# Optimization experiments

Hardware: AMD Instinct MI355X
Metric: run time of the kernel (lower is better)

Reference implementation:

```python
import jax, jax.numpy as jnp
import numpy as np

NUM_VIEW = 300
NUM_ANGLE = 12
NUM_DEPTH = 4
GRASP_MAX_WIDTH = 0.1
B, C, NS, NG = 2, 512, 2048, 2000


def generate_grasp_views(N=NUM_VIEW):
    phi = (np.sqrt(5.0) - 1.0) / 2.0  # fibonacci sphere
    idxs = jnp.arange(N, dtype=jnp.float32)
    Z = (2.0 * idxs + 1.0) / N - 1.0
    r = jnp.sqrt(jnp.maximum(1.0 - Z * Z, 0.0))
    X = r * jnp.cos(2.0 * jnp.pi * idxs * phi)
    Y = r * jnp.sin(2.0 * jnp.pi * idxs * phi)
    return jnp.stack([X, Y, Z], -1)  # [N,3]


def viewpoint_params_to_matrix(towards, angle):
    # towards [...,3], angle [...]
    ax = towards
    zero = jnp.zeros_like(ax[..., 0])
    ay = jnp.stack([-ax[..., 1], ax[..., 0], zero], -1)
    ynorm = jnp.linalg.norm(ay, axis=-1, keepdims=True)
    ay = jnp.where(ynorm == 0, jnp.array([0.0, 1.0, 0.0], ax.dtype), ay)
    ax = ax / jnp.linalg.norm(ax, axis=-1, keepdims=True)
    ay = ay / jnp.linalg.norm(ay, axis=-1, keepdims=True)
    az = jnp.cross(ax, ay)
    c, s = jnp.cos(angle), jnp.sin(angle)
    one = jnp.ones_like(c)
    R1 = jnp.stack([one, zero * 0 + jnp.zeros_like(c), jnp.zeros_like(c),
                    jnp.zeros_like(c), c, -s,
                    jnp.zeros_like(c), s, c], -1).reshape(angle.shape + (3, 3))
    R2 = jnp.stack([ax, ay, az], -1)  # axes as columns
    return R2 @ R1


def conv1d(x, w, b):
    # 1x1 Conv1d == channel matmul. x [B,Ci,N], w [Co,Ci]
    return jnp.einsum('oi,bin->bon', w, x) + b[None, :, None]


def knn1(q, ref):
    # K=1 nearest neighbor indices of q [Nq,3] in ref [Nr,3]
    d = (jnp.sum(q * q, -1, keepdims=True) + jnp.sum(ref * ref, -1)[None, :]
         - 2.0 * q @ ref.T)
    return jnp.argmin(d, axis=-1)


def normalize_tensor(t, eps=1e-8):
    mx = jnp.max(t, -1, keepdims=True)
    mn = jnp.min(t, -1, keepdims=True)
    return (t - mn) / (mx - mn + eps)


def _process_one(seed_xyz, pose, gpoints, gscores, gwidths, views, views_rot):
    R, t = pose[:, :3], pose[:, 3]
    gp_trans = gpoints @ R.T + t                      # [Ng,3]
    gv_trans = views @ R.T                            # [V,3]
    gv_rot_trans = jnp.einsum('ij,vjk->vik', R, views_rot)  # [V,3,3]
    view_inds = knn1(views, gv_trans)                 # [V]
    gv_rot_trans = gv_rot_trans[view_inds]            # [V,3,3]
    nn_inds = knn1(seed_xyz, gp_trans)                # [Ns]
    gp_out = gp_trans[nn_inds]                        # [Ns,3]
    # gather seed dim first (Ns<Ng) then reindex views; axes independent
    sc = gscores[nn_inds][:, view_inds]               # [Ns,V,A,D]
    wd = gwidths[nn_inds][:, view_inds]
    rot = jnp.broadcast_to(gv_rot_trans[None], (seed_xyz.shape[0],) + gv_rot_trans.shape)
    return gp_out, rot, sc, wd


def setup_inputs() -> dict:
    key = jax.random.key(0)
    ks = jax.random.split(key, 16)
    seed_features = jax.random.normal(ks[0], (B, C, NS), jnp.float32)
    point_clouds = jax.random.normal(ks[1], (B, NS, 3), jnp.float32) * 0.2
    Rq = np.linalg.qr(np.asarray(jax.random.normal(ks[2], (B, 3, 3))))[0].astype(np.float32)
    trans = jax.random.normal(ks[3], (B, 3, 1), jnp.float32) * 0.1
    object_pose = jnp.concatenate([jnp.asarray(Rq), trans], -1)  # [B,3,4]
    grasp_points = jax.random.normal(ks[4], (B, NG, 3), jnp.float32) * 0.2
    grasp_labels = jax.random.uniform(ks[5], (B, NG, NUM_VIEW, NUM_ANGLE, NUM_DEPTH)) * 1.2 - 0.2
    grasp_offsets = jax.random.uniform(ks[6], (B, NG, NUM_VIEW, NUM_ANGLE, NUM_DEPTH)) * 0.15
    w = lambda k, co, ci: jax.random.normal(k, (co, ci), jnp.float32) * 0.05
    bz = lambda co: jnp.zeros((co,), jnp.float32)
    return {
        'seed_features': seed_features, 'point_clouds': point_clouds,
        'object_pose': object_pose, 'grasp_points': grasp_points,
        'grasp_labels': grasp_labels, 'grasp_offsets': grasp_offsets,
        'aw1_w': w(ks[7], C, C), 'aw1_b': bz(C),
        'aw2_w': w(ks[8], C, C), 'aw2_b': bz(C),
        'aw3_w': w(ks[9], NUM_VIEW, C), 'aw3_b': bz(NUM_VIEW),
        'sw1_w': w(ks[10], C, C), 'sw1_b': bz(C),
        'sw2_w': w(ks[11], NUM_DEPTH * NUM_ANGLE * 2, C), 'sw2_b': bz(NUM_DEPTH * NUM_ANGLE * 2),
    }


def reference(seed_features, point_clouds, object_pose, grasp_points,
              grasp_labels, grasp_offsets, aw1_w, aw1_b, aw2_w, aw2_b,
              aw3_w, aw3_b, sw1_w, sw1_b, sw2_w, sw2_b):
    Bx, Cx, Ns = seed_features.shape
    # --- ApproachNet (eval branch) ---
    res = jax.nn.relu(conv1d(seed_features, aw1_w, aw1_b))
    res = jax.nn.relu(conv1d(res, aw2_w, aw2_b))
    view_scores = conv1d(res, aw3_w, aw3_b).transpose(0, 2, 1)  # [B,Ns,V]
    top_view_inds = jnp.argmax(view_scores, -1)                 # [B,Ns]
    views = generate_grasp_views(NUM_VIEW)
    vp_xyz = views[top_view_inds]                               # [B,Ns,3]
    vp_rot = viewpoint_params_to_matrix(-vp_xyz, jnp.zeros(vp_xyz.shape[:-1], vp_xyz.dtype))
    # --- SWADNet ---
    f = jax.nn.relu(conv1d(res, sw1_w, sw1_b))
    f = conv1d(f, sw2_w, sw2_b)
    f = f.reshape(Bx, 2, NUM_ANGLE, NUM_DEPTH, Ns).transpose(0, 1, 4, 2, 3)
    grasp_score_pred = f[:, 0]   # [B,Ns,A,D]
    grasp_width_pred = f[:, 1]
    # --- process_grasp_labels (vmapped over batch) ---
    views_rot = viewpoint_params_to_matrix(-views, jnp.zeros((NUM_VIEW,), views.dtype))
    gp, rot, sc, wd = jax.vmap(_process_one, in_axes=(0, 0, 0, 0, 0, None, None))(
        point_clouds, object_pose, grasp_points, grasp_labels, grasp_offsets, views, views_rot)
    gmask = (sc <= 0.6) & (sc > 0)
    graspness = normalize_tensor(
        gmask.astype(jnp.float32).reshape(Bx, Ns, NUM_VIEW, -1).mean(-1))  # [B,Ns,V]
    label_mask = (sc > 0) & (wd <= GRASP_MAX_WIDTH)
    sc = jnp.where(label_mask, sc, 0.0)
    # --- match_grasp_view_and_label ---
    bi = jnp.arange(Bx)[:, None]
    ni = jnp.arange(Ns)[None, :]
    top_rot = rot[bi, ni, top_view_inds]  # [B,Ns,3,3]
    top_sc = sc[bi, ni, top_view_inds]    # [B,Ns,A,D]
    top_wd = wd[bi, ni, top_view_inds]
    u_max = jnp.max(top_sc)
    po = top_sc > 0
    safe = jnp.where(po, top_sc, 1.0)
    u_min = jnp.min(jnp.where(po, top_sc, jnp.inf))
    new_sc = jnp.log(u_max / safe) / (jnp.log(u_max / u_min) + 1e-8)
    top_sc = jnp.where(po, new_sc, top_sc)
    return (view_scores, vp_rot, grasp_score_pred, grasp_width_pred,
            top_rot, top_sc, top_wd, graspness, gp)
```

## Files before the change

### kernel.cpp

```cpp
#include <hip/hip_runtime.h>
#include <math.h>

#define NV 300
#define NA 12
#define ND 4
#define NB 2
#define NC 512
#define NSD 2048
#define NGP 2000
#define ROWLEN 14400

__global__ void k_setup(float* __restrict__ views, float* __restrict__ views_rot,
                        int* __restrict__ mmx) {
  int i = threadIdx.x;
  if (i == 0) { mmx[0] = 0; mmx[1] = 0x7f800000; }
  if (i >= NV) return;
  float fi = (float)i;
  float Z = (2.0f * fi + 1.0f) / 300.0f - 1.0f;
  float r = sqrtf(fmaxf(1.0f - Z * Z, 0.0f));
  float ang = (6.28318530717958647692f * fi) * 0.61803398874989484820f;
  float X = r * cosf(ang);
  float Y = r * sinf(ang);
  views[i * 3 + 0] = X; views[i * 3 + 1] = Y; views[i * 3 + 2] = Z;
  float ax0 = -X, ax1 = -Y, ax2 = -Z;
  float ay0 = -ax1, ay1 = ax0, ay2 = 0.f;
  float ynorm = sqrtf(ay0 * ay0 + ay1 * ay1 + ay2 * ay2);
  if (ynorm == 0.f) { ay0 = 0.f; ay1 = 1.f; ay2 = 0.f; }
  float an = sqrtf(ax0 * ax0 + ax1 * ax1 + ax2 * ax2);
  ax0 /= an; ax1 /= an; ax2 /= an;
  float ayn = sqrtf(ay0 * ay0 + ay1 * ay1 + ay2 * ay2);
  ay0 /= ayn; ay1 /= ayn; ay2 /= ayn;
  float az0 = ax1 * ay2 - ax2 * ay1;
  float az1 = ax2 * ay0 - ax0 * ay2;
  float az2 = ax0 * ay1 - ax1 * ay0;
  float* m = views_rot + i * 9;
  m[0] = ax0; m[1] = ay0; m[2] = az0;
  m[3] = ax1; m[4] = ay1; m[5] = az1;
  m[6] = ax2; m[7] = ay2; m[8] = az2;
}

__global__ void __launch_bounds__(512) k_batch_setup(
    const float* __restrict__ pose, const float* __restrict__ views,
    const float* __restrict__ views_rot, int* __restrict__ view_inds,
    float* __restrict__ Rsel) {
  int b = blockIdx.x, tid = threadIdx.x;
  __shared__ float R[9];
  __shared__ float gv[NV][3];
  __shared__ float gvr[NV];
  if (tid < 9) R[tid] = pose[b * 12 + (tid / 3) * 4 + (tid % 3)];
  __syncthreads();
  if (tid < NV) {
    float vx = views[tid * 3], vy = views[tid * 3 + 1], vz = views[tid * 3 + 2];
    float x = R[0] * vx + R[1] * vy + R[2] * vz;
    float y = R[3] * vx + R[4] * vy + R[5] * vz;
    float z = R[6] * vx + R[7] * vy + R[8] * vz;
    gv[tid][0] = x; gv[tid][1] = y; gv[tid][2] = z;
    gvr[tid] = x * x + y * y + z * z;
  }
  __syncthreads();
  if (tid < NV) {
    float qx = views[tid * 3], qy = views[tid * 3 + 1], qz = views[tid * 3 + 2];
    float qq = qx * qx + qy * qy + qz * qz;
    float best = INFINITY; int bi = 0;
    for (int u = 0; u < NV; u++) {
      float dot = qx * gv[u][0] + qy * gv[u][1] + qz * gv[u][2];
      float d = qq + gvr[u] - 2.f * dot;
      if (d < best) { best = d; bi = u; }
    }
    view_inds[b * NV + tid] = bi;
    const float* vr = views_rot + bi * 9;
    float* o = Rsel + (b * NV + tid) * 9;
    for (int i = 0; i < 3; i++)
      for (int j = 0; j < 3; j++)
        o[i * 3 + j] = R[i * 3 + 0] * vr[0 + j] + R[i * 3 + 1] * vr[3 + j] + R[i * 3 + 2] * vr[6 + j];
  }
}

__global__ void k_gp_trans(const float* __restrict__ pose,
                           const float* __restrict__ gpoints,
                           float4* __restrict__ gpt4) {
  int idx = blockIdx.x * 256 + threadIdx.x;
  if (idx >= NB * NGP) return;
  int b = idx / NGP;
  const float* P = pose + b * 12;
  float px = gpoints[(size_t)idx * 3 + 0];
  float py = gpoints[(size_t)idx * 3 + 1];
  float pz = gpoints[(size_t)idx * 3 + 2];
  float x = P[0] * px + P[1] * py + P[2] * pz + P[3];
  float y = P[4] * px + P[5] * py + P[6] * pz + P[7];
  float z = P[8] * px + P[9] * py + P[10] * pz + P[11];
  gpt4[idx] = make_float4(x, y, z, x * x + y * y + z * z);
}

__global__ void __launch_bounds__(256) k_nn(
    const float* __restrict__ pc, const float4* __restrict__ gpt4,
    int* __restrict__ nn_inds, float* __restrict__ out_gp) {
  int b = blockIdx.y;
  int s0 = blockIdx.x * 32;
  int tid = threadIdx.x;
  __shared__ float4 pts[NGP];
  for (int i = tid; i < NGP; i += 256) pts[i] = gpt4[b * NGP + i];
  __syncthreads();
  int sl = tid & 31, chunk = tid >> 5;
  int s = s0 + sl;
  float qx = pc[((size_t)b * NSD + s) * 3 + 0];
  float qy = pc[((size_t)b * NSD + s) * 3 + 1];
  float qz = pc[((size_t)b * NSD + s) * 3 + 2];
  float qq = qx * qx + qy * qy + qz * qz;
  int i0 = chunk * 250;
  float best = INFINITY; int bi = i0;
  for (int i = i0; i < i0 + 250; i++) {
    float4 p = pts[i];
    float d = qq + p.w - 2.f * (qx * p.x + qy * p.y + qz * p.z);
    if (d < best) { best = d; bi = i; }
  }
  __shared__ float rb[8][33];
  __shared__ int ri[8][33];
  rb[chunk][sl] = best; ri[chunk][sl] = bi;
  __syncthreads();
  if (tid < 32) {
    float bb = INFINITY; int ii = 0;
    for (int c = 0; c < 8; c++) {
      float v = rb[c][tid];
      if (v < bb) { bb = v; ii = ri[c][tid]; }
    }
    nn_inds[b * NSD + s0 + tid] = ii;
    float4 p = pts[ii];
    out_gp[((size_t)b * NSD + s0 + tid) * 3 + 0] = p.x;
    out_gp[((size_t)b * NSD + s0 + tid) * 3 + 1] = p.y;
    out_gp[((size_t)b * NSD + s0 + tid) * 3 + 2] = p.z;
  }
}

template <bool RELU, bool GUARD_M>
__global__ void __launch_bounds__(256) gemm128(
    const float* __restrict__ W, const float* __restrict__ X,
    const float* __restrict__ bias, float* __restrict__ Y,
    int O, int Cin, int N) {
  int b = blockIdx.z;
  const float* Xb = X + (size_t)b * Cin * N;
  float* Yb = Y + (size_t)b * O * N;
  int m0 = blockIdx.y * 128, n0 = blockIdx.x * 64;
  __shared__ float As[16][132];
  __shared__ float Bs[16][64];
  int tid = threadIdx.x;
  int mW = tid >> 1;
  int kW = (tid & 1) * 8;
  int kX = tid >> 4, nX = (tid & 15) * 4;
  int ty = tid >> 4, tx = tid & 15;
  bool okm = !GUARD_M || (m0 + mW) < O;
  float4 a0, a1, bv;
  {
    const float* wp = &W[(size_t)(m0 + mW) * Cin + kW];
    a0 = okm ? *(const float4*)wp : make_float4(0.f, 0.f, 0.f, 0.f);
    a1 = okm ? *(const float4*)(wp + 4) : make_float4(0.f, 0.f, 0.f, 0.f);
    bv = *(const float4*)&Xb[(size_t)kX * N + n0 + nX];
  }
  float acc[8][4] = {};
  for (int k0 = 0; k0 < Cin; k0 += 16) {
    __syncthreads();
    As[kW + 0][mW] = a0.x; As[kW + 1][mW] = a0.y;
    As[kW + 2][mW] = a0.z; As[kW + 3][mW] = a0.w;
    As[kW + 4][mW] = a1.x; As[kW + 5][mW] = a1.y;
    As[kW + 6][mW] = a1.z; As[kW + 7][mW] = a1.w;
    *(float4*)&Bs[kX][nX] = bv;
    __syncthreads();
    if (k0 + 16 < Cin) {
      const float* wp = &W[(size_t)(m0 + mW) * Cin + k0 + 16 + kW];
      a0 = okm ? *(const float4*)wp : make_float4(0.f, 0.f, 0.f, 0.f);
      a1 = okm ? *(const float4*)(wp + 4) : make_float4(0.f, 0.f, 0.f, 0.f);
      bv = *(const float4*)&Xb[(size_t)(k0 + 16 + kX) * N + n0 + nX];
    }
#pragma unroll
    for (int kk = 0; kk < 16; kk++) {
      float4 x0 = *(const float4*)&As[kk][ty * 8];
      float4 x1 = *(const float4*)&As[kk][ty * 8 + 4];
      float4 y = *(const float4*)&Bs[kk][tx * 4];
      acc[0][0] = fmaf(x0.x, y.x, acc[0][0]); acc[0][1] = fmaf(x0.x, y.y, acc[0][1]);
      acc[0][2] = fmaf(x0.x, y.z, acc[0][2]); acc[0][3] = fmaf(x0.x, y.w, acc[0][3]);
      acc[1][0] = fmaf(x0.y, y.x, acc[1][0]); acc[1][1] = fmaf(x0.y, y.y, acc[1][1]);
      acc[1][2] = fmaf(x0.y, y.z, acc[1][2]); acc[1][3] = fmaf(x0.y, y.w, acc[1][3]);
      acc[2][0] = fmaf(x0.z, y.x, acc[2][0]); acc[2][1] = fmaf(x0.z, y.y, acc[2][1]);
      acc[2][2] = fmaf(x0.z, y.z, acc[2][2]); acc[2][3] = fmaf(x0.z, y.w, acc[2][3]);
      acc[3][0] = fmaf(x0.w, y.x, acc[3][0]); acc[3][1] = fmaf(x0.w, y.y, acc[3][1]);
      acc[3][2] = fmaf(x0.w, y.z, acc[3][2]); acc[3][3] = fmaf(x0.w, y.w, acc[3][3]);
      acc[4][0] = fmaf(x1.x, y.x, acc[4][0]); acc[4][1] = fmaf(x1.x, y.y, acc[4][1]);
      acc[4][2] = fmaf(x1.x, y.z, acc[4][2]); acc[4][3] = fmaf(x1.x, y.w, acc[4][3]);
      acc[5][0] = fmaf(x1.y, y.x, acc[5][0]); acc[5][1] = fmaf(x1.y, y.y, acc[5][1]);
      acc[5][2] = fmaf(x1.y, y.z, acc[5][2]); acc[5][3] = fmaf(x1.y, y.w, acc[5][3]);
      acc[6][0] = fmaf(x1.z, y.x, acc[6][0]); acc[6][1] = fmaf(x1.z, y.y, acc[6][1]);
      acc[6][2] = fmaf(x1.z, y.z, acc[6][2]); acc[6][3] = fmaf(x1.z, y.w, acc[6][3]);
      acc[7][0] = fmaf(x1.w, y.x, acc[7][0]); acc[7][1] = fmaf(x1.w, y.y, acc[7][1]);
      acc[7][2] = fmaf(x1.w, y.z, acc[7][2]); acc[7][3] = fmaf(x1.w, y.w, acc[7][3]);
    }
  }
#pragma unroll
  for (int i = 0; i < 8; i++) {
    int m = m0 + ty * 8 + i;
    if (GUARD_M && m >= O) break;
    float bi = bias[m];
    float4 v;
    v.x = acc[i][0] + bi; v.y = acc[i][1] + bi;
    v.z = acc[i][2] + bi; v.w = acc[i][3] + bi;
    if (RELU) {
      v.x = fmaxf(v.x, 0.f); v.y = fmaxf(v.y, 0.f);
      v.z = fmaxf(v.z, 0.f); v.w = fmaxf(v.w, 0.f);
    }
    *(float4*)&Yb[(size_t)m * N + n0 + (tx << 2)] = v;
  }
}

template <bool RELU, bool GUARD_M>
__global__ void __launch_bounds__(256) gemm_k(
    const float* __restrict__ W, const float* __restrict__ X,
    const float* __restrict__ bias, float* __restrict__ Y,
    int O, int Cin, int N) {
  int b = blockIdx.z;
  const float* Xb = X + (size_t)b * Cin * N;
  float* Yb = Y + (size_t)b * O * N;
  int m0 = blockIdx.y * 64, n0 = blockIdx.x * 64;
  __shared__ float As[16][68];
  __shared__ float Bs[16][64];
  int tid = threadIdx.x;
  int mW = tid >> 2, kW = (tid & 3) * 4;
  int kX = tid >> 4, nX = (tid & 15) * 4;
  int ty = tid >> 4, tx = tid & 15;
  float acc[4][4] = {};
  for (int k0 = 0; k0 < Cin; k0 += 16) {
    float4 wv;
    if (!GUARD_M || (m0 + mW) < O)
      wv = *(const float4*)&W[(size_t)(m0 + mW) * Cin + k0 + kW];
    else
      wv = make_float4(0.f, 0.f, 0.f, 0.f);
    As[kW + 0][mW] = wv.x; As[kW + 1][mW] = wv.y;
    As[kW + 2][mW] = wv.z; As[kW + 3][mW] = wv.w;
    *(float4*)&Bs[kX][nX] = *(const float4*)&Xb[(size_t)(k0 + kX) * N + n0 + nX];
    __syncthreads();
#pragma unroll
    for (int kk = 0; kk < 16; kk++) {
      float4 a = *(const float4*)&As[kk][ty << 2];
      float4 bv = *(const float4*)&Bs[kk][tx << 2];
      acc[0][0] = fmaf(a.x, bv.x, acc[0][0]); acc[0][1] = fmaf(a.x, bv.y, acc[0][1]);
      acc[0][2] = fmaf(a.x, bv.z, acc[0][2]); acc[0][3] = fmaf(a.x, bv.w, acc[0][3]);
      acc[1][0] = fmaf(a.y, bv.x, acc[1][0]); acc[1][1] = fmaf(a.y, bv.y, acc[1][1]);
      acc[1][2] = fmaf(a.y, bv.z, acc[1][2]); acc[1][3] = fmaf(a.y, bv.w, acc[1][3]);
      acc[2][0] = fmaf(a.z, bv.x, acc[2][0]); acc[2][1] = fmaf(a.z, bv.y, acc[2][1]);
      acc[2][2] = fmaf(a.z, bv.z, acc[2][2]); acc[2][3] = fmaf(a.z, bv.w, acc[2][3]);
      acc[3][0] = fmaf(a.w, bv.x, acc[3][0]); acc[3][1] = fmaf(a.w, bv.y, acc[3][1]);
      acc[3][2] = fmaf(a.w, bv.z, acc[3][2]); acc[3][3] = fmaf(a.w, bv.w, acc[3][3]);
    }
    __syncthreads();
  }
#pragma unroll
  for (int i = 0; i < 4; i++) {
    int m = m0 + ty * 4 + i;
    if (GUARD_M && m >= O) break;
    float bi = bias[m];
    float4 v;
    v.x = acc[i][0] + bi; v.y = acc[i][1] + bi;
    v.z = acc[i][2] + bi; v.w = acc[i][3] + bi;
    if (RELU) {
      v.x = fmaxf(v.x, 0.f); v.y = fmaxf(v.y, 0.f);
      v.z = fmaxf(v.z, 0.f); v.w = fmaxf(v.w, 0.f);
    }
    *(float4*)&Yb[(size_t)m * N + n0 + (tx << 2)] = v;
  }
}

__global__ void __launch_bounds__(256) k_argmax(
    const float* __restrict__ vs_t, const float* __restrict__ views_rot,
    const float* __restrict__ Rsel, int* __restrict__ tv_inds,
    float* __restrict__ o_vprot, float* __restrict__ o_trot) {
  int b = blockIdx.y;
  int n = blockIdx.x * 256 + threadIdx.x;
  const float* src = vs_t + (size_t)b * NV * NSD + n;
  float best = src[0]; int bi = 0;
  for (int v = 1; v < NV; v++) {
    float val = src[(size_t)v * NSD];
    if (val > best) { best = val; bi = v; }
  }
  tv_inds[b * NSD + n] = bi;
  const float* vr = views_rot + bi * 9;
  float* o1 = o_vprot + ((size_t)b * NSD + n) * 9;
  const float* rs = Rsel + (b * NV + bi) * 9;
  float* o4 = o_trot + ((size_t)b * NSD + n) * 9;
#pragma unroll
  for (int i = 0; i < 9; i++) { o1[i] = vr[i]; o4[i] = rs[i]; }
}

__global__ void k_transpose_vs(const float* __restrict__ vs_t, float* __restrict__ out) {
  __shared__ float tile[32][33];
  int b = blockIdx.z;
  int v0 = blockIdx.x * 32, n0 = blockIdx.y * 32;
  const float* src = vs_t + (size_t)b * NV * NSD;
  for (int i = threadIdx.y; i < 32; i += 8) {
    int v = v0 + i;
    if (v < NV) tile[i][threadIdx.x] = src[(size_t)v * NSD + n0 + threadIdx.x];
  }
  __syncthreads();
  for (int i = threadIdx.y; i < 32; i += 8) {
    int n = n0 + i;
    int v = v0 + threadIdx.x;
    if (v < NV) out[((size_t)b * NSD + n) * NV + v] = tile[threadIdx.x][i];
  }
}

__global__ void __launch_bounds__(256) k_f2(const float* __restrict__ f2,
                                            float* __restrict__ gsp,
                                            float* __restrict__ gwp) {
  __shared__ float tile[96][65];
  int b = blockIdx.y, n0 = blockIdx.x * 64;
  const float* src = f2 + (size_t)b * 96 * NSD;
  for (int idx = threadIdx.x; idx < 96 * 64; idx += 256) {
    int ch = idx >> 6, j = idx & 63;
    tile[ch][j] = src[(size_t)ch * NSD + n0 + j];
  }
  __syncthreads();
  for (int idx = threadIdx.x; idx < 64 * 48; idx += 256) {
    int j = idx / 48, ad = idx % 48;
    size_t o = ((size_t)b * NSD + n0 + j) * 48 + ad;
    gsp[o] = tile[ad][j];
    gwp[o] = tile[48 + ad][j];
  }
}

__global__ void __launch_bounds__(256) k_grasp(
    const float* __restrict__ gscores, const float* __restrict__ goffsets,
    const int* __restrict__ nn_inds, const int* __restrict__ tv_inds,
    const int* __restrict__ view_inds, float* __restrict__ o_grsp,
    float* __restrict__ o_twd, float* __restrict__ raw) {
  int b = blockIdx.y, s = blockIdx.x, tid = threadIdx.x;
  __shared__ int vi[NV];
  for (int v = tid; v < NV; v += 256) vi[v] = view_inds[b * NV + v];
  __syncthreads();
  int nn = nn_inds[b * NSD + s];
  int tv = tv_inds[b * NSD + s];
  int vit = vi[tv];
  const float* srow = gscores + ((size_t)(b * NGP + nn)) * ROWLEN;
  const float* wrow = goffsets + ((size_t)(b * NGP + nn)) * ROWLEN;
  if (tid < 48) {
    float sc = srow[vit * 48 + tid];
    float wd = wrow[vit * 48 + tid];
    bool m = (sc > 0.f) && (wd <= 0.1f);
    o_twd[((size_t)b * NSD + s) * 48 + tid] = wd;
    raw[((size_t)b * NSD + s) * 48 + tid] = m ? sc : 0.f;
  }
  __shared__ float g[NV];
  for (int v = tid; v < NV; v += 256) {
    int vv = vi[v];
    const float4* p = (const float4*)(srow + vv * 48);
    int cnt = 0;
#pragma unroll
    for (int q = 0; q < 12; q++) {
      float4 x = p[q];
      cnt += (x.x > 0.f && x.x <= 0.6f);
      cnt += (x.y > 0.f && x.y <= 0.6f);
      cnt += (x.z > 0.f && x.z <= 0.6f);
      cnt += (x.w > 0.f && x.w <= 0.6f);
    }
    g[v] = (float)cnt / 48.0f;
  }
  __syncthreads();
  float mx = -INFINITY, mn = INFINITY;
  for (int v = tid; v < NV; v += 256) { mx = fmaxf(mx, g[v]); mn = fminf(mn, g[v]); }
  for (int off = 32; off; off >>= 1) {
    mx = fmaxf(mx, __shfl_down(mx, off));
    mn = fminf(mn, __shfl_down(mn, off));
  }
  __shared__ float wmx[4], wmn[4];
  int wid = tid >> 6, lane = tid & 63;
  if (lane == 0) { wmx[wid] = mx; wmn[wid] = mn; }
  __syncthreads();
  if (tid == 0) {
    mx = fmaxf(fmaxf(wmx[0], wmx[1]), fmaxf(wmx[2], wmx[3]));
    mn = fminf(fminf(wmn[0], wmn[1]), fminf(wmn[2], wmn[3]));
    wmx[0] = mx; wmn[0] = mn;
  }
  __syncthreads();
  mx = wmx[0]; mn = wmn[0];
  float denom = mx - mn + 1e-8f;
  float* og = o_grsp + ((size_t)b * NSD + s) * NV;
  for (int v = tid; v < NV; v += 256) og[v] = (g[v] - mn) / denom;
}

__global__ void __launch_bounds__(256) k_reduce(const float* __restrict__ raw,
                                                int n, int* __restrict__ mmx) {
  float mx = -INFINITY, mn = INFINITY;
  for (int i = blockIdx.x * 256 + threadIdx.x; i < n; i += gridDim.x * 256) {
    float v = raw[i];
    mx = fmaxf(mx, v);
    if (v > 0.f) mn = fminf(mn, v);
  }
  for (int off = 32; off; off >>= 1) {
    mx = fmaxf(mx, __shfl_down(mx, off));
    mn = fminf(mn, __shfl_down(mn, off));
  }
  __shared__ float smx[4], smn[4];
  int wid = threadIdx.x >> 6, lane = threadIdx.x & 63;
  if (lane == 0) { smx[wid] = mx; smn[wid] = mn; }
  __syncthreads();
  if (threadIdx.x == 0) {
    mx = fmaxf(fmaxf(smx[0], smx[1]), fmaxf(smx[2], smx[3]));
    mn = fminf(fminf(smn[0], smn[1]), fminf(smn[2], smn[3]));
    atomicMax(&mmx[0], __float_as_int(mx));
    if (mn != INFINITY) atomicMin(&mmx[1], __float_as_int(mn));
  }
}

__global__ void k_topsc(const float* __restrict__ raw, const int* __restrict__ mmx,
                        float* __restrict__ out, int n) {
  int i = blockIdx.x * 256 + threadIdx.x;
  if (i >= n) return;
  float sc = raw[i];
  float umax = __int_as_float(mmx[0]);
  float umin = __int_as_float(mmx[1]);
  float denom = logf(umax / umin) + 1e-8f;
  float val = logf(umax / sc) / denom;
  out[i] = (sc > 0.f) ? val : sc;
}

extern "C" void kernel_launch(void* const* d_in, const int* in_sizes, int n_in,
                              void* d_out, int out_size, void* d_ws, size_t ws_size,
                              hipStream_t stream) {
  const float* seed_features = (const float*)d_in[0];
  const float* point_clouds  = (const float*)d_in[1];
  const float* object_pose   = (const float*)d_in[2];
  const float* grasp_points  = (const float*)d_in[3];
  const float* grasp_labels  = (const float*)d_in[4];
  const float* grasp_offsets = (const float*)d_in[5];
  const float* aw1_w = (const float*)d_in[6];
  const float* aw1_b = (const float*)d_in[7];
  const float* aw2_w = (const float*)d_in[8];
  const float* aw2_b = (const float*)d_in[9];
  const float* aw3_w = (const float*)d_in[10];
  const float* aw3_b = (const float*)d_in[11];
  const float* sw1_w = (const float*)d_in[12];
  const float* sw1_b = (const float*)d_in[13];
  const float* sw2_w = (const float*)d_in[14];
  const float* sw2_b = (const float*)d_in[15];

  float* out = (float*)d_out;
  float* o_vs    = out;
  float* o_vprot = o_vs + NB * NSD * NV;
  float* o_gsp   = o_vprot + NB * NSD * 9;
  float* o_gwp   = o_gsp + NB * NSD * 48;
  float* o_trot  = o_gwp + NB * NSD * 48;
  float* o_tsc   = o_trot + NB * NSD * 9;
  float* o_twd   = o_tsc + NB * NSD * 48;
  float* o_grsp  = o_twd + NB * NSD * 48;
  float* o_gp    = o_grsp + NB * NSD * NV;

  float* w = (float*)d_ws;
  float* res1 = w; w += NB * NC * NSD;
  float* res2 = w; w += NB * NC * NSD;
  float* vs_t = w; w += NB * NV * NSD;
  float* f2   = w; w += NB * 96 * NSD;
  float* views = w; w += 960;
  float* views_rot = w; w += 2720;
  float4* gpt4 = (float4*)w; w += NB * NGP * 4;
  float* Rsel = w; w += NB * NV * 9;
  float* raw  = w; w += NB * NSD * 48;
  int* view_inds = (int*)w; w += NB * NV;
  int* nn_inds   = (int*)w; w += NB * NSD;
  int* tv_inds   = (int*)w; w += NB * NSD;
  int* mmx       = (int*)w; w += 8;

  k_setup<<<1, 512, 0, stream>>>(views, views_rot, mmx);
  k_batch_setup<<<NB, 512, 0, stream>>>(object_pose, views, views_rot, view_inds, Rsel);
  k_gp_trans<<<(NB * NGP + 255) / 256, 256, 0, stream>>>(object_pose, grasp_points, gpt4);
  k_nn<<<dim3(NSD / 32, NB), 256, 0, stream>>>(point_clouds, gpt4, nn_inds, o_gp);

  gemm128<true, false><<<dim3(NSD / 64, NC / 128, NB), 256, 0, stream>>>(
      aw1_w, seed_features, aw1_b, res1, NC, NC, NSD);
  gemm128<true, false><<<dim3(NSD / 64, NC / 128, NB), 256, 0, stream>>>(
      aw2_w, res1, aw2_b, res2, NC, NC, NSD);
  gemm128<false, true><<<dim3(NSD / 64, (NV + 127) / 128, NB), 256, 0, stream>>>(
      aw3_w, res2, aw3_b, vs_t, NV, NC, NSD);
  gemm128<true, false><<<dim3(NSD / 64, NC / 128, NB), 256, 0, stream>>>(
      sw1_w, res2, sw1_b, res1, NC, NC, NSD);
  gemm_k<false, true><<<dim3(NSD / 64, 2, NB), 256, 0, stream>>>(
      sw2_w, res1, sw2_b, f2, 96, NC, NSD);

  k_argmax<<<dim3(NSD / 256, NB), 256, 0, stream>>>(vs_t, views_rot, Rsel, tv_inds,
                                                    o_vprot, o_trot);
  k_transpose_vs<<<dim3((NV + 31) / 32, NSD / 32, NB), dim3(32, 8), 0, stream>>>(vs_t, o_vs);
  k_f2<<<dim3(NSD / 64, NB), 256, 0, stream>>>(f2, o_gsp, o_gwp);
  k_grasp<<<dim3(NSD, NB), 256, 0, stream>>>(grasp_labels, grasp_offsets, nn_inds,
                                             tv_inds, view_inds, o_grsp, o_twd, raw);
  k_reduce<<<256, 256, 0, stream>>>(raw, NB * NSD * 48, mmx);
  k_topsc<<<(NB * NSD * 48 + 255) / 256, 256, 0, stream>>>(raw, mmx, o_tsc, NB * NSD * 48);
}
```

Baseline: 659.4 us.

## Replace FP32 SIMT GEMMs with split-bf16x3 MFMA GEMMs

Four of the large 1x1-conv GEMMs move from FP32 FMA loops to bf16 MFMA instructions. Each weight and activation is split into three bf16 parts (high, mid, low), and six cross-product MFMAs are accumulated to keep near-FP32 accuracy. New kernels do the weight splitting and a transposed activation splitting before each GEMM, which adds memory traffic and extra launches. The aw3 GEMM is reordered to run after sw1 so it can reuse the split copy of res2.

```diff
diff --git a/kernel.cpp b/kernel.cpp
--- a/kernel.cpp
+++ b/kernel.cpp
@@ -1,5 +1,6 @@
 #include <hip/hip_runtime.h>
 #include <math.h>
+#include <stdint.h>
 
 #define NV 300
 #define NA 12
@@ -9,6 +10,27 @@
 #define NSD 2048
 #define NGP 2000
 #define ROWLEN 14400
+
+#define XPLANE ((size_t)NB * NSD * NC)
+
+typedef __attribute__((ext_vector_type(8))) short bf16x8;
+typedef __attribute__((ext_vector_type(4))) float f32x4;
+
+__device__ __forceinline__ unsigned short f2bf(float f) {
+  unsigned u = __float_as_uint(f);
+  return (unsigned short)((u + 0x7fffu + ((u >> 16) & 1u)) >> 16);
+}
+__device__ __forceinline__ float bf2f(unsigned short s) {
+  return __uint_as_float(((unsigned)s) << 16);
+}
+__device__ __forceinline__ void split3(float x, short& h, short& m, short& l) {
+  unsigned short hb = f2bf(x);
+  float r1 = x - bf2f(hb);
+  unsigned short mb = f2bf(r1);
+  float r2 = r1 - bf2f(mb);
+  unsigned short lb = f2bf(r2);
+  h = (short)hb; m = (short)mb; l = (short)lb;
+}
 
 __global__ void k_setup(float* __restrict__ views, float* __restrict__ views_rot,
                         int* __restrict__ mmx) {
@@ -132,81 +154,135 @@
   }
 }
 
-template <bool RELU, bool GUARD_M>
-__global__ void __launch_bounds__(256) gemm128(
-    const float* __restrict__ W, const float* __restrict__ X,
-    const float* __restrict__ bias, float* __restrict__ Y,
-    int O, int Cin, int N) {
+__global__ void __launch_bounds__(256) k_wsplit(
+    const float* __restrict__ w0, const float* __restrict__ w1,
+    const float* __restrict__ w2, const float* __restrict__ w3,
+    short* __restrict__ WP) {
+  int mat = blockIdx.y;
+  const float* src = (mat == 0) ? w0 : (mat == 1) ? w1 : (mat == 2) ? w2 : w3;
+  int rows = (mat == 3) ? 300 : 512;
+  int po = (mat == 3) ? 384 : 512;
+  size_t base = (size_t)mat * (3 * 512 * 512);
+  int pl = po * 512;
+  int idx = blockIdx.x * 1024 + threadIdx.x * 4;
+  if (idx >= pl) return;
+  short4 h = make_short4(0, 0, 0, 0), m = h, l = h;
+  if (idx < rows * 512) {
+    float4 x = *(const float4*)&src[idx];
+    split3(x.x, h.x, m.x, l.x);
+    split3(x.y, h.y, m.y, l.y);
+    split3(x.z, h.z, m.z, l.z);
+    split3(x.w, h.w, m.w, l.w);
+  }
+  short* dst = WP + base;
+  *(short4*)&dst[idx] = h;
+  *(short4*)&dst[(size_t)pl + idx] = m;
+  *(short4*)&dst[2 * (size_t)pl + idx] = l;
+}
+
+__global__ void __launch_bounds__(256) k_xsplit(const float* __restrict__ X,
+                                                short* __restrict__ XP) {
   int b = blockIdx.z;
-  const float* Xb = X + (size_t)b * Cin * N;
-  float* Yb = Y + (size_t)b * O * N;
-  int m0 = blockIdx.y * 128, n0 = blockIdx.x * 64;
-  __shared__ float As[16][132];
-  __shared__ float Bs[16][64];
+  int n0 = blockIdx.x * 32, k0 = blockIdx.y * 32;
+  __shared__ float t[32][36];
   int tid = threadIdx.x;
-  int mW = tid >> 1;
-  int kW = (tid & 1) * 8;
-  int kX = tid >> 4, nX = (tid & 15) * 4;
-  int ty = tid >> 4, tx = tid & 15;
-  bool okm = !GUARD_M || (m0 + mW) < O;
-  float4 a0, a1, bv;
+  int r = tid >> 3, c4 = (tid & 7) << 2;
+  *(float4*)&t[r][c4] =
+      *(const float4*)&X[((size_t)b * NC + k0 + r) * NSD + n0 + c4];
+  __syncthreads();
+  int nr = tid >> 3, ks = (tid & 7) << 2;
+  short ha[4], ma[4], la[4];
+#pragma unroll
+  for (int j = 0; j < 4; j++) {
+    float x = t[ks + j][nr];
+    split3(x, ha[j], ma[j], la[j]);
+  }
+  size_t o = ((size_t)b * NSD + n0 + nr) * NC + k0 + ks;
+  *(short4*)&XP[o] = make_short4(ha[0], ha[1], ha[2], ha[3]);
+  *(short4*)&XP[XPLANE + o] = make_short4(ma[0], ma[1], ma[2], ma[3]);
+  *(short4*)&XP[2 * XPLANE + o] = make_short4(la[0], la[1], la[2], la[3]);
+}
+
+template <bool RELU, int O, int PO>
+__global__ void __launch_bounds__(256) k_mfma(
+    const short* __restrict__ Wm, const short* __restrict__ XPb,
+    const float* __restrict__ bias, float* __restrict__ Y) {
+  const size_t PPL = (size_t)PO * NC;
+  int b = blockIdx.z;
+  int n0 = blockIdx.x * 64, m0 = blockIdx.y * 128;
+  int tid = threadIdx.x;
+  int wave = tid >> 6, lane = tid & 63;
+  int wr = wave >> 1, wc = wave & 1;
+  int lr = lane & 15, j8 = lane >> 4;
+  __shared__ short Bs[2][3][64][40];
+  int srow = tid >> 2, schk = tid & 3;
+  const short* xsrc = XPb + ((size_t)b * NSD + n0 + srow) * NC + schk * 8;
+  const short* wbase = Wm + (size_t)(m0 + wr * 64 + lr) * NC + j8 * 8;
+  f32x4 acc[4][2] = {};
   {
-    const float* wp = &W[(size_t)(m0 + mW) * Cin + kW];
-    a0 = okm ? *(const float4*)wp : make_float4(0.f, 0.f, 0.f, 0.f);
-    a1 = okm ? *(const float4*)(wp + 4) : make_float4(0.f, 0.f, 0.f, 0.f);
-    bv = *(const float4*)&Xb[(size_t)kX * N + n0 + nX];
-  }
-  float acc[8][4] = {};
-  for (int k0 = 0; k0 < Cin; k0 += 16) {
+    int4 s0 = *(const int4*)(xsrc);
+    int4 s1 = *(const int4*)(xsrc + XPLANE);
+    int4 s2 = *(const int4*)(xsrc + 2 * XPLANE);
+    *(int4*)&Bs[0][0][srow][schk * 8] = s0;
+    *(int4*)&Bs[0][1][srow][schk * 8] = s1;
+    *(int4*)&Bs[0][2][srow][schk * 8] = s2;
+  }
+  __syncthreads();
+  int cur = 0;
+  for (int kk = 0; kk < NC; kk += 32) {
+    bf16x8 a[3][4];
+#pragma unroll
+    for (int p = 0; p < 3; p++)
+#pragma unroll
+      for (int mf = 0; mf < 4; mf++)
+        a[p][mf] = *(const bf16x8*)(wbase + p * PPL + (size_t)(mf * 16) * NC + kk);
+    bf16x8 bq[3][2];
+#pragma unroll
+    for (int q = 0; q < 3; q++)
+#pragma unroll
+      for (int nf = 0; nf < 2; nf++)
+        bq[q][nf] = *(const bf16x8*)&Bs[cur][q][wc * 32 + nf * 16 + lr][j8 * 8];
+    if (kk + 32 < NC) {
+      const short* s = xsrc + kk + 32;
+      int4 s0 = *(const int4*)(s);
+      int4 s1 = *(const int4*)(s + XPLANE);
+      int4 s2 = *(const int4*)(s + 2 * XPLANE);
+      *(int4*)&Bs[cur ^ 1][0][srow][schk * 8] = s0;
+      *(int4*)&Bs[cur ^ 1][1][srow][schk * 8] = s1;
+      *(int4*)&Bs[cur ^ 1][2][srow][schk * 8] = s2;
+    }
+#pragma unroll
+    for (int mf = 0; mf < 4; mf++)
+#pragma unroll
+      for (int nf = 0; nf < 2; nf++) {
+        f32x4 c = acc[mf][nf];
+        c = __builtin_amdgcn_mfma_f32_16x16x32_bf16(a[0][mf], bq[0][nf], c, 0, 0, 0);
+        c = __builtin_amdgcn_mfma_f32_16x16x32_bf16(a[0][mf], bq[1][nf], c, 0, 0, 0);
+        c = __builtin_amdgcn_mfma_f32_16x16x32_bf16(a[1][mf], bq[0][nf], c, 0, 0, 0);
+        c = __builtin_amdgcn_mfma_f32_16x16x32_bf16(a[0][mf], bq[2][nf], c, 0, 0, 0);
+        c = __builtin_amdgcn_mfma_f32_16x16x32_bf16(a[2][mf], bq[0][nf], c, 0, 0, 0);
+        c = __builtin_amdgcn_mfma_f32_16x16x32_bf16(a[1][mf], bq[1][nf], c, 0, 0, 0);
+        acc[mf][nf] = c;
+      }
     __syncthreads();
-    As[kW + 0][mW] = a0.x; As[kW + 1][mW] = a0.y;
-    As[kW + 2][mW] = a0.z; As[kW + 3][mW] = a0.w;
-    As[kW + 4][mW] = a1.x; As[kW + 5][mW] = a1.y;
-    As[kW + 6][mW] = a1.z; As[kW + 7][mW] = a1.w;
-    *(float4*)&Bs[kX][nX] = bv;
-    __syncthreads();
-    if (k0 + 16 < Cin) {
-      const float* wp = &W[(size_t)(m0 + mW) * Cin + k0 + 16 + kW];
-      a0 = okm ? *(const float4*)wp : make_float4(0.f, 0.f, 0.f, 0.f);
-      a1 = okm ? *(const float4*)(wp + 4) : make_float4(0.f, 0.f, 0.f, 0.f);
-      bv = *(const float4*)&Xb[(size_t)(k0 + 16 + kX) * N + n0 + nX];
-    }
-#pragma unroll
-    for (int kk = 0; kk < 16; kk++) {
-      float4 x0 = *(const float4*)&As[kk][ty * 8];
-      float4 x1 = *(const float4*)&As[kk][ty * 8 + 4];
-      float4 y = *(const float4*)&Bs[kk][tx * 4];
-      acc[0][0] = fmaf(x0.x, y.x, acc[0][0]); acc[0][1] = fmaf(x0.x, y.y, acc[0][1]);
-      acc[0][2] = fmaf(x0.x, y.z, acc[0][2]); acc[0][3] = fmaf(x0.x, y.w, acc[0][3]);
-      acc[1][0] = fmaf(x0.y, y.x, acc[1][0]); acc[1][1] = fmaf(x0.y, y.y, acc[1][1]);
-      acc[1][2] = fmaf(x0.y, y.z, acc[1][2]); acc[1][3] = fmaf(x0.y, y.w, acc[1][3]);
-      acc[2][0] = fmaf(x0.z, y.x, acc[2][0]); acc[2][1] = fmaf(x0.z, y.y, acc[2][1]);
-      acc[2][2] = fmaf(x0.z, y.z, acc[2][2]); acc[2][3] = fmaf(x0.z, y.w, acc[2][3]);
-      acc[3][0] = fmaf(x0.w, y.x, acc[3][0]); acc[3][1] = fmaf(x0.w, y.y, acc[3][1]);
-      acc[3][2] = fmaf(x0.w, y.z, acc[3][2]); acc[3][3] = fmaf(x0.w, y.w, acc[3][3]);
-      acc[4][0] = fmaf(x1.x, y.x, acc[4][0]); acc[4][1] = fmaf(x1.x, y.y, acc[4][1]);
-      acc[4][2] = fmaf(x1.x, y.z, acc[4][2]); acc[4][3] = fmaf(x1.x, y.w, acc[4][3]);
-      acc[5][0] = fmaf(x1.y, y.x, acc[5][0]); acc[5][1] = fmaf(x1.y, y.y, acc[5][1]);
-      acc[5][2] = fmaf(x1.y, y.z, acc[5][2]); acc[5][3] = fmaf(x1.y, y.w, acc[5][3]);
-      acc[6][0] = fmaf(x1.z, y.x, acc[6][0]); acc[6][1] = fmaf(x1.z, y.y, acc[6][1]);
-      acc[6][2] = fmaf(x1.z, y.z, acc[6][2]); acc[6][3] = fmaf(x1.z, y.w, acc[6][3]);
-      acc[7][0] = fmaf(x1.w, y.x, acc[7][0]); acc[7][1] = fmaf(x1.w, y.y, acc[7][1]);
-      acc[7][2] = fmaf(x1.w, y.z, acc[7][2]); acc[7][3] = fmaf(x1.w, y.w, acc[7][3]);
-    }
-  }
-#pragma unroll
-  for (int i = 0; i < 8; i++) {
-    int m = m0 + ty * 8 + i;
-    if (GUARD_M && m >= O) break;
-    float bi = bias[m];
-    float4 v;
-    v.x = acc[i][0] + bi; v.y = acc[i][1] + bi;
-    v.z = acc[i][2] + bi; v.w = acc[i][3] + bi;
-    if (RELU) {
-      v.x = fmaxf(v.x, 0.f); v.y = fmaxf(v.y, 0.f);
-      v.z = fmaxf(v.z, 0.f); v.w = fmaxf(v.w, 0.f);
-    }
-    *(float4*)&Yb[(size_t)m * N + n0 + (tx << 2)] = v;
+    cur ^= 1;
+  }
+  float* Yb = Y + (size_t)b * O * NSD;
+#pragma unroll
+  for (int mf = 0; mf < 4; mf++) {
+#pragma unroll
+    for (int j = 0; j < 4; j++) {
+      int ro = m0 + wr * 64 + mf * 16 + j8 * 4 + j;
+      if (PO == O || ro < O) {
+        float bv = bias[ro];
+#pragma unroll
+        for (int nf = 0; nf < 2; nf++) {
+          float v = acc[mf][nf][j] + bv;
+          if (RELU) v = fmaxf(v, 0.f);
+          Yb[(size_t)ro * NSD + n0 + wc * 32 + nf * 16 + lr] = v;
+        }
+      }
+    }
   }
 }
 
@@ -464,20 +540,23 @@
   int* nn_inds   = (int*)w; w += NB * NSD;
   int* tv_inds   = (int*)w; w += NB * NSD;
   int* mmx       = (int*)w; w += 8;
+  w = (float*)(((uintptr_t)w + 15) & ~(uintptr_t)15);
+  short* WP = (short*)w; w += 1474560;
+  short* XP = (short*)w; w += 3145728;
 
   k_setup<<<1, 512, 0, stream>>>(views, views_rot, mmx);
   k_batch_setup<<<NB, 512, 0, stream>>>(object_pose, views, views_rot, view_inds, Rsel);
   k_gp_trans<<<(NB * NGP + 255) / 256, 256, 0, stream>>>(object_pose, grasp_points, gpt4);
   k_nn<<<dim3(NSD / 32, NB), 256, 0, stream>>>(point_clouds, gpt4, nn_inds, o_gp);
 
-  gemm128<true, false><<<dim3(NSD / 64, NC / 128, NB), 256, 0, stream>>>(
-      aw1_w, seed_features, aw1_b, res1, NC, NC, NSD);
-  gemm128<true, false><<<dim3(NSD / 64, NC / 128, NB), 256, 0, stream>>>(
-      aw2_w, res1, aw2_b, res2, NC, NC, NSD);
-  gemm128<false, true><<<dim3(NSD / 64, (NV + 127) / 128, NB), 256, 0, stream>>>(
-      aw3_w, res2, aw3_b, vs_t, NV, NC, NSD);
-  gemm128<true, false><<<dim3(NSD / 64, NC / 128, NB), 256, 0, stream>>>(
-      sw1_w, res2, sw1_b, res1, NC, NC, NSD);
+  k_wsplit<<<dim3(256, 4), 256, 0, stream>>>(aw1_w, aw2_w, sw1_w, aw3_w, WP);
+  k_xsplit<<<dim3(NSD / 32, NC / 32, NB), 256, 0, stream>>>(seed_features, XP);
+  k_mfma<true, 512, 512><<<dim3(NSD / 64, 4, NB), 256, 0, stream>>>(WP, XP, aw1_b, res1);
+  k_xsplit<<<dim3(NSD / 32, NC / 32, NB), 256, 0, stream>>>(res1, XP);
+  k_mfma<true, 512, 512><<<dim3(NSD / 64, 4, NB), 256, 0, stream>>>(WP + 786432, XP, aw2_b, res2);
+  k_xsplit<<<dim3(NSD / 32, NC / 32, NB), 256, 0, stream>>>(res2, XP);
+  k_mfma<true, 512, 512><<<dim3(NSD / 64, 4, NB), 256, 0, stream>>>(WP + 1572864, XP, sw1_b, res1);
+  k_mfma<false, 300, 384><<<dim3(NSD / 64, 3, NB), 256, 0, stream>>>(WP + 2359296, XP, aw3_b, vs_t);
   gemm_k<false, true><<<dim3(NSD / 64, 2, NB), 256, 0, stream>>>(
       sw2_w, res1, sw2_b, f2, 96, NC, NSD);
 
```

After: 682.9 us. 3.6% more time.

## Fuse setup, point transform, sw2 transpose, and view argmax/transpose kernels

Applied to the files above, without the earlier changes.

Merges the view-generation kernel into the per-batch setup kernel and moves the grasp-point transform into the NN kernel's shared-memory load. The sw2 GEMM now writes its output transposed directly into the grasp score/width buffers, and the argmax and view-score transpose are combined into one tiled kernel. This cuts several launches and intermediate global buffers. The cost is redundant view computation per batch block, and the transform is repeated in every NN block.

```diff
diff --git a/kernel.cpp b/kernel.cpp
--- a/kernel.cpp
+++ b/kernel.cpp
@@ -1,5 +1,6 @@
 #include <hip/hip_runtime.h>
 #include <math.h>
+#include <stdint.h>
 
 #define NV 300
 #define NA 12
@@ -10,47 +11,48 @@
 #define NGP 2000
 #define ROWLEN 14400
 
-__global__ void k_setup(float* __restrict__ views, float* __restrict__ views_rot,
-                        int* __restrict__ mmx) {
-  int i = threadIdx.x;
-  if (i == 0) { mmx[0] = 0; mmx[1] = 0x7f800000; }
-  if (i >= NV) return;
-  float fi = (float)i;
-  float Z = (2.0f * fi + 1.0f) / 300.0f - 1.0f;
-  float r = sqrtf(fmaxf(1.0f - Z * Z, 0.0f));
-  float ang = (6.28318530717958647692f * fi) * 0.61803398874989484820f;
-  float X = r * cosf(ang);
-  float Y = r * sinf(ang);
-  views[i * 3 + 0] = X; views[i * 3 + 1] = Y; views[i * 3 + 2] = Z;
-  float ax0 = -X, ax1 = -Y, ax2 = -Z;
-  float ay0 = -ax1, ay1 = ax0, ay2 = 0.f;
-  float ynorm = sqrtf(ay0 * ay0 + ay1 * ay1 + ay2 * ay2);
-  if (ynorm == 0.f) { ay0 = 0.f; ay1 = 1.f; ay2 = 0.f; }
-  float an = sqrtf(ax0 * ax0 + ax1 * ax1 + ax2 * ax2);
-  ax0 /= an; ax1 /= an; ax2 /= an;
-  float ayn = sqrtf(ay0 * ay0 + ay1 * ay1 + ay2 * ay2);
-  ay0 /= ayn; ay1 /= ayn; ay2 /= ayn;
-  float az0 = ax1 * ay2 - ax2 * ay1;
-  float az1 = ax2 * ay0 - ax0 * ay2;
-  float az2 = ax0 * ay1 - ax1 * ay0;
-  float* m = views_rot + i * 9;
-  m[0] = ax0; m[1] = ay0; m[2] = az0;
-  m[3] = ax1; m[4] = ay1; m[5] = az1;
-  m[6] = ax2; m[7] = ay2; m[8] = az2;
-}
-
-__global__ void __launch_bounds__(512) k_batch_setup(
-    const float* __restrict__ pose, const float* __restrict__ views,
-    const float* __restrict__ views_rot, int* __restrict__ view_inds,
-    float* __restrict__ Rsel) {
+__global__ void __launch_bounds__(512) k_setup_all(
+    const float* __restrict__ pose, float* __restrict__ views_rot_g,
+    int* __restrict__ view_inds, float* __restrict__ Rsel, int* __restrict__ mmx) {
   int b = blockIdx.x, tid = threadIdx.x;
+  __shared__ float sv[NV][3];
+  __shared__ float svr[NV][9];
   __shared__ float R[9];
   __shared__ float gv[NV][3];
   __shared__ float gvr[NV];
+  if (b == 0 && tid == 0) { mmx[0] = 0; mmx[1] = 0x7f800000; }
   if (tid < 9) R[tid] = pose[b * 12 + (tid / 3) * 4 + (tid % 3)];
-  __syncthreads();
   if (tid < NV) {
-    float vx = views[tid * 3], vy = views[tid * 3 + 1], vz = views[tid * 3 + 2];
+    float fi = (float)tid;
+    float Z = (2.0f * fi + 1.0f) / 300.0f - 1.0f;
+    float r = sqrtf(fmaxf(1.0f - Z * Z, 0.0f));
+    float ang = (6.28318530717958647692f * fi) * 0.61803398874989484820f;
+    float X = r * cosf(ang);
+    float Y = r * sinf(ang);
+    sv[tid][0] = X; sv[tid][1] = Y; sv[tid][2] = Z;
+    float ax0 = -X, ax1 = -Y, ax2 = -Z;
+    float ay0 = -ax1, ay1 = ax0, ay2 = 0.f;
+    float ynorm = sqrtf(ay0 * ay0 + ay1 * ay1 + ay2 * ay2);
+    if (ynorm == 0.f) { ay0 = 0.f; ay1 = 1.f; ay2 = 0.f; }
+    float an = sqrtf(ax0 * ax0 + ax1 * ax1 + ax2 * ax2);
+    ax0 /= an; ax1 /= an; ax2 /= an;
+    float ayn = sqrtf(ay0 * ay0 + ay1 * ay1 + ay2 * ay2);
+    ay0 /= ayn; ay1 /= ayn; ay2 /= ayn;
+    float az0 = ax1 * ay2 - ax2 * ay1;
+    float az1 = ax2 * ay0 - ax0 * ay2;
+    float az2 = ax0 * ay1 - ax1 * ay0;
+    svr[tid][0] = ax0; svr[tid][1] = ay0; svr[tid][2] = az0;
+    svr[tid][3] = ax1; svr[tid][4] = ay1; svr[tid][5] = az1;
+    svr[tid][6] = ax2; svr[tid][7] = ay2; svr[tid][8] = az2;
+    if (b == 0) {
+      float* m = views_rot_g + tid * 9;
+#pragma unroll
+      for (int i = 0; i < 9; i++) m[i] = svr[tid][i];
+    }
+  }
+  __syncthreads();
+  if (tid < NV) {
+    float vx = sv[tid][0], vy = sv[tid][1], vz = sv[tid][2];
     float x = R[0] * vx + R[1] * vy + R[2] * vz;
     float y = R[3] * vx + R[4] * vy + R[5] * vz;
     float z = R[6] * vx + R[7] * vy + R[8] * vz;
@@ -59,7 +61,7 @@
   }
   __syncthreads();
   if (tid < NV) {
-    float qx = views[tid * 3], qy = views[tid * 3 + 1], qz = views[tid * 3 + 2];
+    float qx = sv[tid][0], qy = sv[tid][1], qz = sv[tid][2];
     float qq = qx * qx + qy * qy + qz * qz;
     float best = INFINITY; int bi = 0;
     for (int u = 0; u < NV; u++) {
@@ -68,7 +70,7 @@
       if (d < best) { best = d; bi = u; }
     }
     view_inds[b * NV + tid] = bi;
-    const float* vr = views_rot + bi * 9;
+    const float* vr = svr[bi];
     float* o = Rsel + (b * NV + tid) * 9;
     for (int i = 0; i < 3; i++)
       for (int j = 0; j < 3; j++)
@@ -76,30 +78,26 @@
   }
 }
 
-__global__ void k_gp_trans(const float* __restrict__ pose,
-                           const float* __restrict__ gpoints,
-                           float4* __restrict__ gpt4) {
-  int idx = blockIdx.x * 256 + threadIdx.x;
-  if (idx >= NB * NGP) return;
-  int b = idx / NGP;
-  const float* P = pose + b * 12;
-  float px = gpoints[(size_t)idx * 3 + 0];
-  float py = gpoints[(size_t)idx * 3 + 1];
-  float pz = gpoints[(size_t)idx * 3 + 2];
-  float x = P[0] * px + P[1] * py + P[2] * pz + P[3];
-  float y = P[4] * px + P[5] * py + P[6] * pz + P[7];
-  float z = P[8] * px + P[9] * py + P[10] * pz + P[11];
-  gpt4[idx] = make_float4(x, y, z, x * x + y * y + z * z);
-}
-
 __global__ void __launch_bounds__(256) k_nn(
-    const float* __restrict__ pc, const float4* __restrict__ gpt4,
-    int* __restrict__ nn_inds, float* __restrict__ out_gp) {
+    const float* __restrict__ pc, const float* __restrict__ pose,
+    const float* __restrict__ gpoints, int* __restrict__ nn_inds,
+    float* __restrict__ out_gp) {
   int b = blockIdx.y;
   int s0 = blockIdx.x * 32;
   int tid = threadIdx.x;
   __shared__ float4 pts[NGP];
-  for (int i = tid; i < NGP; i += 256) pts[i] = gpt4[b * NGP + i];
+  __shared__ float P[12];
+  if (tid < 12) P[tid] = pose[b * 12 + tid];
+  __syncthreads();
+  for (int i = tid; i < NGP; i += 256) {
+    float px = gpoints[((size_t)b * NGP + i) * 3 + 0];
+    float py = gpoints[((size_t)b * NGP + i) * 3 + 1];
+    float pz = gpoints[((size_t)b * NGP + i) * 3 + 2];
+    float x = P[0] * px + P[1] * py + P[2] * pz + P[3];
+    float y = P[4] * px + P[5] * py + P[6] * pz + P[7];
+    float z = P[8] * px + P[9] * py + P[10] * pz + P[11];
+    pts[i] = make_float4(x, y, z, x * x + y * y + z * z);
+  }
   __syncthreads();
   int sl = tid & 31, chunk = tid >> 5;
   int s = s0 + sl;
@@ -210,14 +208,13 @@
   }
 }
 
-template <bool RELU, bool GUARD_M>
-__global__ void __launch_bounds__(256) gemm_k(
+__global__ void __launch_bounds__(256) gemm_sw2(
     const float* __restrict__ W, const float* __restrict__ X,
-    const float* __restrict__ bias, float* __restrict__ Y,
-    int O, int Cin, int N) {
+    const float* __restrict__ bias, float* __restrict__ gsp,
+    float* __restrict__ gwp) {
+  const int O = 96, Cin = NC, N = NSD;
   int b = blockIdx.z;
   const float* Xb = X + (size_t)b * Cin * N;
-  float* Yb = Y + (size_t)b * O * N;
   int m0 = blockIdx.y * 64, n0 = blockIdx.x * 64;
   __shared__ float As[16][68];
   __shared__ float Bs[16][64];
@@ -228,7 +225,7 @@
   float acc[4][4] = {};
   for (int k0 = 0; k0 < Cin; k0 += 16) {
     float4 wv;
-    if (!GUARD_M || (m0 + mW) < O)
+    if ((m0 + mW) < O)
       wv = *(const float4*)&W[(size_t)(m0 + mW) * Cin + k0 + kW];
     else
       wv = make_float4(0.f, 0.f, 0.f, 0.f);
@@ -251,76 +248,67 @@
     }
     __syncthreads();
   }
-#pragma unroll
-  for (int i = 0; i < 4; i++) {
-    int m = m0 + ty * 4 + i;
-    if (GUARD_M && m >= O) break;
-    float bi = bias[m];
-    float4 v;
-    v.x = acc[i][0] + bi; v.y = acc[i][1] + bi;
-    v.z = acc[i][2] + bi; v.w = acc[i][3] + bi;
-    if (RELU) {
-      v.x = fmaxf(v.x, 0.f); v.y = fmaxf(v.y, 0.f);
-      v.z = fmaxf(v.z, 0.f); v.w = fmaxf(v.w, 0.f);
-    }
-    *(float4*)&Yb[(size_t)m * N + n0 + (tx << 2)] = v;
-  }
-}
-
-__global__ void __launch_bounds__(256) k_argmax(
+  int m = m0 + ty * 4;
+  if (m < O) {
+    float b0 = bias[m], b1 = bias[m + 1], b2 = bias[m + 2], b3 = bias[m + 3];
+#pragma unroll
+    for (int j = 0; j < 4; j++) {
+      int n = n0 + (tx << 2) + j;
+      float4 v;
+      v.x = acc[0][j] + b0; v.y = acc[1][j] + b1;
+      v.z = acc[2][j] + b2; v.w = acc[3][j] + b3;
+      size_t base = ((size_t)b * NSD + n) * 48;
+      if (m < 48) *(float4*)&gsp[base + m] = v;
+      else        *(float4*)&gwp[base + m - 48] = v;
+    }
+  }
+}
+
+__global__ void __launch_bounds__(256) k_view(
     const float* __restrict__ vs_t, const float* __restrict__ views_rot,
     const float* __restrict__ Rsel, int* __restrict__ tv_inds,
-    float* __restrict__ o_vprot, float* __restrict__ o_trot) {
-  int b = blockIdx.y;
-  int n = blockIdx.x * 256 + threadIdx.x;
-  const float* src = vs_t + (size_t)b * NV * NSD + n;
-  float best = src[0]; int bi = 0;
-  for (int v = 1; v < NV; v++) {
-    float val = src[(size_t)v * NSD];
-    if (val > best) { best = val; bi = v; }
-  }
-  tv_inds[b * NSD + n] = bi;
-  const float* vr = views_rot + bi * 9;
-  float* o1 = o_vprot + ((size_t)b * NSD + n) * 9;
-  const float* rs = Rsel + (b * NV + bi) * 9;
-  float* o4 = o_trot + ((size_t)b * NSD + n) * 9;
-#pragma unroll
-  for (int i = 0; i < 9; i++) { o1[i] = vr[i]; o4[i] = rs[i]; }
-}
-
-__global__ void k_transpose_vs(const float* __restrict__ vs_t, float* __restrict__ out) {
+    float* __restrict__ o_vs, float* __restrict__ o_vprot,
+    float* __restrict__ o_trot) {
+  int b = blockIdx.y, n0 = blockIdx.x * 32;
+  int tx = threadIdx.x, ty = threadIdx.y;
   __shared__ float tile[32][33];
-  int b = blockIdx.z;
-  int v0 = blockIdx.x * 32, n0 = blockIdx.y * 32;
+  __shared__ float bval[8][32];
+  __shared__ int bidx[8][32];
   const float* src = vs_t + (size_t)b * NV * NSD;
-  for (int i = threadIdx.y; i < 32; i += 8) {
-    int v = v0 + i;
-    if (v < NV) tile[i][threadIdx.x] = src[(size_t)v * NSD + n0 + threadIdx.x];
-  }
-  __syncthreads();
-  for (int i = threadIdx.y; i < 32; i += 8) {
-    int n = n0 + i;
-    int v = v0 + threadIdx.x;
-    if (v < NV) out[((size_t)b * NSD + n) * NV + v] = tile[threadIdx.x][i];
-  }
-}
-
-__global__ void __launch_bounds__(256) k_f2(const float* __restrict__ f2,
-                                            float* __restrict__ gsp,
-                                            float* __restrict__ gwp) {
-  __shared__ float tile[96][65];
-  int b = blockIdx.y, n0 = blockIdx.x * 64;
-  const float* src = f2 + (size_t)b * 96 * NSD;
-  for (int idx = threadIdx.x; idx < 96 * 64; idx += 256) {
-    int ch = idx >> 6, j = idx & 63;
-    tile[ch][j] = src[(size_t)ch * NSD + n0 + j];
-  }
-  __syncthreads();
-  for (int idx = threadIdx.x; idx < 64 * 48; idx += 256) {
-    int j = idx / 48, ad = idx % 48;
-    size_t o = ((size_t)b * NSD + n0 + j) * 48 + ad;
-    gsp[o] = tile[ad][j];
-    gwp[o] = tile[48 + ad][j];
+  float best = -INFINITY; int bi = 0;
+  for (int v0 = 0; v0 < NV; v0 += 32) {
+    int vlim = (NV - v0 < 32) ? (NV - v0) : 32;
+    for (int i = ty; i < vlim; i += 8)
+      tile[i][tx] = src[(size_t)(v0 + i) * NSD + n0 + tx];
+    __syncthreads();
+    if (v0 + tx < NV) {
+#pragma unroll
+      for (int j = 0; j < 4; j++) {
+        int nl = ty * 4 + j;
+        o_vs[((size_t)b * NSD + n0 + nl) * NV + v0 + tx] = tile[tx][nl];
+      }
+    }
+    for (int i = ty; i < vlim; i += 8) {
+      float val = tile[i][tx];
+      if (val > best) { best = val; bi = v0 + i; }
+    }
+    __syncthreads();
+  }
+  bval[ty][tx] = best; bidx[ty][tx] = bi;
+  __syncthreads();
+  if (ty == 0) {
+    for (int t = 1; t < 8; t++) {
+      float v = bval[t][tx]; int ii = bidx[t][tx];
+      if (v > best || (v == best && ii < bi)) { best = v; bi = ii; }
+    }
+    int n = n0 + tx;
+    tv_inds[b * NSD + n] = bi;
+    const float* vr = views_rot + bi * 9;
+    const float* rs = Rsel + (b * NV + bi) * 9;
+    float* o1 = o_vprot + ((size_t)b * NSD + n) * 9;
+    float* o4 = o_trot + ((size_t)b * NSD + n) * 9;
+#pragma unroll
+    for (int i = 0; i < 9; i++) { o1[i] = vr[i]; o4[i] = rs[i]; }
   }
 }
 
@@ -454,10 +442,7 @@
   float* res1 = w; w += NB * NC * NSD;
   float* res2 = w; w += NB * NC * NSD;
   float* vs_t = w; w += NB * NV * NSD;
-  float* f2   = w; w += NB * 96 * NSD;
-  float* views = w; w += 960;
   float* views_rot = w; w += 2720;
-  float4* gpt4 = (float4*)w; w += NB * NGP * 4;
   float* Rsel = w; w += NB * NV * 9;
   float* raw  = w; w += NB * NSD * 48;
   int* view_inds = (int*)w; w += NB * NV;
@@ -465,10 +450,9 @@
   int* tv_inds   = (int*)w; w += NB * NSD;
   int* mmx       = (int*)w; w += 8;
 
-  k_setup<<<1, 512, 0, stream>>>(views, views_rot, mmx);
-  k_batch_setup<<<NB, 512, 0, stream>>>(object_pose, views, views_rot, view_inds, Rsel);
-  k_gp_trans<<<(NB * NGP + 255) / 256, 256, 0, stream>>>(object_pose, grasp_points, gpt4);
-  k_nn<<<dim3(NSD / 32, NB), 256, 0, stream>>>(point_clouds, gpt4, nn_inds, o_gp);
+  k_setup_all<<<NB, 512, 0, stream>>>(object_pose, views_rot, view_inds, Rsel, mmx);
+  k_nn<<<dim3(NSD / 32, NB), 256, 0, stream>>>(point_clouds, object_pose, grasp_points,
+                                               nn_inds, o_gp);
 
   gemm128<true, false><<<dim3(NSD / 64, NC / 128, NB), 256, 0, stream>>>(
       aw1_w, seed_features, aw1_b, res1, NC, NC, NSD);
@@ -478,13 +462,10 @@
       aw3_w, res2, aw3_b, vs_t, NV, NC, NSD);
   gemm128<true, false><<<dim3(NSD / 64, NC / 128, NB), 256, 0, stream>>>(
       sw1_w, res2, sw1_b, res1, NC, NC, NSD);
-  gemm_k<false, true><<<dim3(NSD / 64, 2, NB), 256, 0, stream>>>(
-      sw2_w, res1, sw2_b, f2, 96, NC, NSD);
-
-  k_argmax<<<dim3(NSD / 256, NB), 256, 0, stream>>>(vs_t, views_rot, Rsel, tv_inds,
-                                                    o_vprot, o_trot);
-  k_transpose_vs<<<dim3((NV + 31) / 32, NSD / 32, NB), dim3(32, 8), 0, stream>>>(vs_t, o_vs);
-  k_f2<<<dim3(NSD / 64, NB), 256, 0, stream>>>(f2, o_gsp, o_gwp);
+  gemm_sw2<<<dim3(NSD / 64, 2, NB), 256, 0, stream>>>(sw2_w, res1, sw2_b, o_gsp, o_gwp);
+
+  k_view<<<dim3(NSD / 32, NB), dim3(32, 8), 0, stream>>>(
+      vs_t, views_rot, Rsel, tv_inds, o_vs, o_vprot, o_trot);
   k_grasp<<<dim3(NSD, NB), 256, 0, stream>>>(grasp_labels, grasp_offsets, nn_inds,
                                              tv_inds, view_inds, o_grsp, o_twd, raw);
   k_reduce<<<256, 256, 0, stream>>>(raw, NB * NSD * 48, mmx);
```

Result: no change. 647.6 us (-1.8%).
